# Performance work log

Measured on AMD Instinct MI355X. Metric: run time of the kernel, lower is better.

## Reference

```python
import jax, jax.numpy as jnp
import numpy as np

N_G, E_G = 76800, 307200   # gg: line graph over bonds
N_L, E_L = 38400, 153600   # lg: atom graph; E_L == 2*N_G
B = 64                     # number of molecules (equal-sized subgraphs)
H = 8                      # attention heads
BOND, ATOM, IN_E, FE1 = 40, 92, 10, 36


def _egat_layer(nfeats, efeats, src, dst, N, W_node, b_node, W_ni, W_nj, W_fij, attn, bias, Fn, Fe):
    # edge scores: gather + add (u_add_v) + edge proj + bias, leaky_relu
    f_edge = (nfeats @ W_ni)[src] + (nfeats @ W_nj)[dst] + efeats @ W_fij + bias
    f_out = jax.nn.leaky_relu(f_edge).reshape(-1, H, Fe)         # [E,H,Fe]
    e = jnp.einsum('ehf,hf->eh', f_out, attn)                     # [E,H]
    # edge softmax over incoming edges of each destination node
    m = jax.lax.stop_gradient(jax.ops.segment_max(e, dst, num_segments=N))
    ex = jnp.exp(e - m[dst])
    a = ex / jax.ops.segment_sum(ex, dst, num_segments=N)[dst]    # [E,H]
    h = (nfeats @ W_node + b_node).reshape(-1, H, Fn)             # [N,H,Fn]
    h_out = jax.ops.segment_sum(h[src] * a[:, :, None], dst, num_segments=N)
    return h_out, f_out


def setup_inputs() -> dict:
    key = jax.random.key(0)
    ks = iter(jax.random.split(key, 64))
    def lin(i, o):
        return jax.random.normal(next(ks), (i, o), jnp.float32) * (1.0 / np.sqrt(i))
    inp = {}
    inp['gg_src'] = jax.random.randint(next(ks), (E_G,), 0, N_G, jnp.int32)
    inp['gg_dst'] = jnp.concatenate([jnp.arange(N_G, dtype=jnp.int32),
                                     jax.random.randint(next(ks), (E_G - N_G,), 0, N_G, jnp.int32)])
    inp['gg_nfeat'] = jax.random.normal(next(ks), (N_G, BOND), jnp.float32)
    inp['gg_efeat'] = jax.random.normal(next(ks), (E_G, IN_E), jnp.float32)
    inp['lg_src'] = jax.random.randint(next(ks), (E_L,), 0, N_L, jnp.int32)
    inp['lg_dst'] = jnp.concatenate([jnp.arange(N_L, dtype=jnp.int32),
                                     jax.random.randint(next(ks), (E_L - N_L,), 0, N_L, jnp.int32)])
    inp['lg_nfeat'] = jax.random.normal(next(ks), (N_L, ATOM), jnp.float32)
    inp['lg_efeat'] = jax.random.normal(next(ks), (E_L, BOND), jnp.float32)
    # layer1 (on gg): in_node=BOND, in_edge=IN_E, out_node=BOND, out_edge=FE1
    inp['W_node1'] = lin(BOND, H * BOND); inp['b_node1'] = jnp.zeros((H * BOND,), jnp.float32)
    inp['W_ni1'] = lin(BOND, H * FE1); inp['W_nj1'] = lin(BOND, H * FE1)
    inp['W_fij1'] = lin(IN_E, H * FE1)
    inp['attn1'] = jax.random.normal(next(ks), (H, FE1), jnp.float32) * 0.1
    inp['bias1'] = jnp.zeros((H * FE1,), jnp.float32)
    # layers 2a/2b (on lg): in_node=ATOM, in_edge=BOND, out_node=ATOM, out_edge=BOND
    for sfx in ('2a', '2b'):
        inp['W_node' + sfx] = lin(ATOM, H * ATOM); inp['b_node' + sfx] = jnp.zeros((H * ATOM,), jnp.float32)
        inp['W_ni' + sfx] = lin(ATOM, H * BOND); inp['W_nj' + sfx] = lin(ATOM, H * BOND)
        inp['W_fij' + sfx] = lin(BOND, H * BOND)
        inp['attn' + sfx] = jax.random.normal(next(ks), (H, BOND), jnp.float32) * 0.1
        inp['bias' + sfx] = jnp.zeros((H * BOND,), jnp.float32)
    # Readout: Linear(128,128) + Sigmoid + Linear(128,1) + Sigmoid
    inp['Wr1'] = lin(ATOM + FE1, 128); inp['br1'] = jnp.zeros((128,), jnp.float32)
    inp['Wr2'] = lin(128, 1); inp['br2'] = jnp.zeros((1,), jnp.float32)
    return inp


def reference(gg_src, gg_dst, gg_nfeat, gg_efeat, lg_src, lg_dst, lg_nfeat, lg_efeat,
              W_node1, b_node1, W_ni1, W_nj1, W_fij1, attn1, bias1,
              W_node2a, b_node2a, W_ni2a, W_nj2a, W_fij2a, attn2a, bias2a,
              W_node2b, b_node2b, W_ni2b, W_nj2b, W_fij2b, attn2b, bias2b,
              Wr1, br1, Wr2, br2):
    # stage 1: EGAT on gg, then sum over heads
    n1, e1 = _egat_layer(gg_nfeat, gg_efeat, gg_src, gg_dst, N_G,
                         W_node1, b_node1, W_ni1, W_nj1, W_fij1, attn1, bias1, BOND, FE1)
    y2n = n1.sum(axis=1)       # [N_G, BOND]
    y22 = e1.sum(axis=1)       # [E_G, FE1]
    # each gg-node feature repeated twice, added to lg edge features
    ef = jnp.repeat(y2n, 2, axis=0) + lg_efeat   # [E_L, BOND]
    nf = lg_nfeat
    nf, e2 = _egat_layer(nf, ef, lg_src, lg_dst, N_L,
                         W_node2a, b_node2a, W_ni2a, W_nj2a, W_fij2a, attn2a, bias2a, ATOM, BOND)
    nf = nf.sum(axis=1); ef = e2.sum(axis=1)
    nf, e2 = _egat_layer(nf, ef, lg_src, lg_dst, N_L,
                         W_node2b, b_node2b, W_ni2b, W_nj2b, W_fij2b, attn2b, bias2b, ATOM, BOND)
    nf = nf.sum(axis=1)
    # per-subgraph average pooling (equal-size subgraphs -> reshape mean).
    # NOTE: original pool_subgraphs(y_22, gg) slices an edge-indexed tensor by node
    # counts (upstream quirk); reproduced exactly by taking the first N_G rows.
    y1 = nf.reshape(B, N_L // B, ATOM).mean(axis=1)          # [B, ATOM]
    y2 = y22[:N_G].reshape(B, N_G // B, FE1).mean(axis=1)    # [B, FE1]
    y = jnp.concatenate([y1, y2], axis=1)                     # [B, 128]
    h = jax.nn.sigmoid(y @ Wr1 + br1)
    return jax.nn.sigmoid(h @ Wr2 + br2)                      # [B, 1]
```

## Files before the change

### kernel.cpp

```cpp
#include <hip/hip_runtime.h>
#include <math.h>

#define NG 76800
#define EG 307200
#define NL 38400
#define EL 153600
#define NB 64
#define NH 8

typedef __attribute__((ext_vector_type(8))) short bf16x8;
typedef __attribute__((ext_vector_type(4))) float f32x4;
typedef unsigned short u16;

__device__ __forceinline__ float sigmoidf(float x) { return 1.f / (1.f + expf(-x)); }
__device__ __forceinline__ u16 f2bf(float x) {
    unsigned u = __float_as_uint(x);
    return (u16)((u + 0x7FFFu + ((u >> 16) & 1u)) >> 16);
}
__device__ __forceinline__ float bf2f(u16 v) { return __uint_as_float(((unsigned)v) << 16); }

__global__ __launch_bounds__(256) void convert_pad_kernel(const float* __restrict__ src,
                                                          u16* __restrict__ dst,
                                                          int M, int K, int Kpad) {
    int i = blockIdx.x * 256 + threadIdx.x;
    if (i >= M * Kpad) return;
    int m = i / Kpad, k = i - m * Kpad;
    dst[i] = (k < K) ? f2bf(src[(size_t)m * K + k]) : (u16)0;
}

__global__ __launch_bounds__(256) void wtrans_kernel(const float* __restrict__ W, int ldw,
                                                     u16* __restrict__ dst,
                                                     int K, int N, int Nalloc, int Kpad) {
    int i = blockIdx.x * 256 + threadIdx.x;
    if (i >= Nalloc * Kpad) return;
    int n = i / Kpad, k = i - n * Kpad;
    dst[i] = (n < N && k < K) ? f2bf(W[(size_t)k * ldw + n]) : (u16)0;
}

__global__ __launch_bounds__(256) void wtrans_hp_kernel(const float* __restrict__ W, int ldw,
                                                        u16* __restrict__ dst,
                                                        int K, int Kpad) {
    int i = blockIdx.x * 256 + threadIdx.x;
    if (i >= 320 * Kpad) return;
    int n = i / Kpad, k = i - n * Kpad;
    int hh = n / 40, f = n - hh * 40;
    float v = (k < K && f < 36) ? W[(size_t)k * ldw + hh * 36 + f] : 0.f;
    dst[i] = f2bf(v);
}

__global__ __launch_bounds__(256) void meta_kernel(const float* __restrict__ attn1,
                                                   const float* __restrict__ bias1,
                                                   const float* __restrict__ b2a,
                                                   const float* __restrict__ b2b,
                                                   float* __restrict__ attn_p1,
                                                   float* __restrict__ bias_cat1,
                                                   float* __restrict__ bias_cat2a,
                                                   float* __restrict__ bias_cat2b) {
    int i = blockIdx.x * 256 + threadIdx.x;
    if (i < 320) {
        int hh = i / 40, f = i - hh * 40;
        attn_p1[i] = (f < 36) ? attn1[hh * 36 + f] : 0.f;
    } else if (i < 960) {
        int j = i - 320;
        float v = 0.f;
        if (j < 320) {
            int hh = j / 40, f = j - hh * 40;
            v = (f < 36) ? bias1[hh * 36 + f] : 0.f;
        }
        bias_cat1[j] = v;
    } else if (i < 1600) {
        int j = i - 960;
        bias_cat2a[j] = (j < 320) ? b2a[j] : 0.f;
    } else if (i < 2240) {
        int j = i - 1600;
        bias_cat2b[j] = (j < 320) ? b2b[j] : 0.f;
    }
}

template <int KPAD>
__global__ __launch_bounds__(256) void gemm_bf_kernel(const u16* __restrict__ A,
                                                      const u16* __restrict__ Wt,
                                                      const float* __restrict__ bias,
                                                      u16* __restrict__ C, int Ncols,
                                                      int Nstride) {
    __shared__ u16 st[4][16 * 72];
    const int m0 = blockIdx.x * 64;
    const int n0 = blockIdx.y * 64;
    const int wv = threadIdx.x >> 6;
    const int lane = threadIdx.x & 63;
    const int q = lane >> 4;
    const int mr = lane & 15;

    const u16* Arow = A + (size_t)(m0 + wv * 16 + mr) * KPAD;
    f32x4 acc[4];
#pragma unroll
    for (int t = 0; t < 4; ++t) acc[t] = (f32x4){0.f, 0.f, 0.f, 0.f};

#pragma unroll
    for (int k0 = 0; k0 < KPAD; k0 += 32) {
        bf16x8 af = *(const bf16x8*)(Arow + k0 + q * 8);
#pragma unroll
        for (int t = 0; t < 4; ++t) {
            bf16x8 bv = *(const bf16x8*)(Wt + (size_t)(n0 + t * 16 + mr) * KPAD + k0 + q * 8);
            acc[t] = __builtin_amdgcn_mfma_f32_16x16x32_bf16(af, bv, acc[t], 0, 0, 0);
        }
    }

    u16* myst = st[wv];
#pragma unroll
    for (int t = 0; t < 4; ++t) {
        const int colme = n0 + t * 16 + mr;
        const float bb = (bias && colme < Ncols) ? bias[colme] : 0.f;
#pragma unroll
        for (int r = 0; r < 4; ++r)
            myst[(q * 4 + r) * 72 + t * 16 + mr] = f2bf(acc[t][r] + bb);
    }
    const int rrow = lane >> 3;
    const int rcol = (lane & 7) * 8;
    bf16x8 v0 = *(const bf16x8*)(myst + rrow * 72 + rcol);
    bf16x8 v1 = *(const bf16x8*)(myst + (rrow + 8) * 72 + rcol);
    const int gcol = n0 + rcol;
    if (gcol < Ncols) {
        const int grow = m0 + wv * 16 + rrow;
        *(bf16x8*)(C + (size_t)grow * Nstride + gcol) = v0;
        *(bf16x8*)(C + (size_t)(grow + 8) * Nstride + gcol) = v1;
    }
}

__global__ __launch_bounds__(256) void ef2a_kernel(const float* __restrict__ lg_ef,
                                                   const float* __restrict__ y2n,
                                                   u16* __restrict__ dst) {
    int i = blockIdx.x * 256 + threadIdx.x;
    if (i >= EL * 64) return;
    int e = i >> 6, c = i & 63;
    dst[i] = (c < 40) ? f2bf(lg_ef[(size_t)e * 40 + c] + y2n[(size_t)(e >> 1) * 40 + c]) : (u16)0;
}

template <int KPAD, int FSMODE>
__global__ __launch_bounds__(256) void pe_edge_kernel(
    const u16* __restrict__ A,
    const u16* __restrict__ Wt,
    const int* __restrict__ src, const int* __restrict__ dst,
    const u16* __restrict__ Pn,
    const float* __restrict__ attn,
    float* __restrict__ esc,
    void* __restrict__ fsum,
    int e0, int CH, int fsumE) {
    __shared__ u16 pe[32][328];
    const int wv = threadIdx.x >> 6;
    const int lane = threadIdx.x & 63;
    const int q = lane >> 4;
    const int mr = lane & 15;
    const int m0 = blockIdx.x * 32;

    {
        const int rg0 = (wv & 1) * 16;
        const int t0 = (wv >> 1) * 10;
        const u16* Arow = A + (size_t)(m0 + rg0 + mr) * KPAD;
        f32x4 acc[10];
#pragma unroll
        for (int t = 0; t < 10; ++t) acc[t] = (f32x4){0.f, 0.f, 0.f, 0.f};
#pragma unroll
        for (int k0 = 0; k0 < KPAD; k0 += 32) {
            bf16x8 af = *(const bf16x8*)(Arow + k0 + q * 8);
#pragma unroll
            for (int t = 0; t < 10; ++t) {
                bf16x8 bv = *(const bf16x8*)(Wt + (size_t)((t0 + t) * 16 + mr) * KPAD + k0 + q * 8);
                acc[t] = __builtin_amdgcn_mfma_f32_16x16x32_bf16(af, bv, acc[t], 0, 0, 0);
            }
        }
#pragma unroll
        for (int t = 0; t < 10; ++t)
#pragma unroll
            for (int r = 0; r < 4; ++r)
                pe[rg0 + q * 4 + r][(t0 + t) * 16 + mr] = f2bf(acc[t][r]);
    }
    __syncthreads();

    const int lc = (lane < 40) ? lane : 39;
    const int h = lc / 5, o = lc - h * 5;
    const int c = h * 40 + o * 8;
    const bool act = (lane < 40);

    float attn_r[8];
#pragma unroll
    for (int j = 0; j < 8; ++j) attn_r[j] = attn[c + j];

    const int row0 = wv * 8;
    int e = e0 + m0 + row0;
    int s = src[e], d = dst[e];
    bf16x8 api = *(const bf16x8*)(Pn + (size_t)s * 640 + c);
    bf16x8 apj = *(const bf16x8*)(Pn + (size_t)d * 640 + 320 + c);

#pragma unroll
    for (int ei = 0; ei < 8; ++ei) {
        bf16x8 napi, napj;
        if (ei < 7) {
            const int ne = e + 1;
            const int ns = src[ne], nd = dst[ne];
            napi = *(const bf16x8*)(Pn + (size_t)ns * 640 + c);
            napj = *(const bf16x8*)(Pn + (size_t)nd * 640 + 320 + c);
        }
        const int row = row0 + ei;
        bf16x8 ape = *(const bf16x8*)(&pe[row][c]);

        float v[8];
        float ehp = 0.f;
#pragma unroll
        for (int j = 0; j < 8; ++j) {
            float x = bf2f((u16)api[j]) + bf2f((u16)apj[j]) + bf2f((u16)ape[j]);
            x = x > 0.f ? x : 0.01f * x;
            v[j] = x;
            ehp += x * attn_r[j];
        }
        float eh = 0.f;
#pragma unroll
        for (int k = 0; k < 5; ++k) eh += __shfl(ehp, h * 5 + k, 64);
        if (act && o == 0) esc[(size_t)e * 8 + h] = eh;

        if (FSMODE != 0 && e < fsumE) {
#pragma unroll
            for (int m = 4; m >= 1; m >>= 1) {
                const int p = (h ^ m) * 5 + o;
#pragma unroll
                for (int j = 0; j < 8; ++j) v[j] += __shfl(v[j], p, 64);
            }
            if (act && h == 0) {
#pragma unroll
                for (int j = 0; j < 8; ++j) {
                    const int f = o * 8 + j;
                    if (FSMODE == 1) {
                        if (f < 36) ((float*)fsum)[(size_t)e * 36 + f] = v[j];
                    } else {
                        ((u16*)fsum)[(size_t)e * 64 + f] = f2bf(v[j]);
                    }
                }
            }
        }
        if (ei < 7) {
            api = napi;
            apj = napj;
        }
        ++e;
    }
}

__global__ __launch_bounds__(256) void hist_kernel(const int* __restrict__ dst,
                                                   int* __restrict__ cnt, int E) {
    int i = blockIdx.x * 256 + threadIdx.x;
    if (i < E) atomicAdd(&cnt[dst[i]], 1);
}

__global__ __launch_bounds__(1024) void scan_block_kernel(const int* __restrict__ cnt,
                                                          int* __restrict__ excl,
                                                          int* __restrict__ bsum, int N) {
    __shared__ int sd[1024];
    const int tid = threadIdx.x;
    const int i = blockIdx.x * 1024 + tid;
    int v = (i < N) ? cnt[i] : 0;
    sd[tid] = v;
    __syncthreads();
    for (int off = 1; off < 1024; off <<= 1) {
        int t = (tid >= off) ? sd[tid - off] : 0;
        __syncthreads();
        sd[tid] += t;
        __syncthreads();
    }
    if (i < N) excl[i] = sd[tid] - v;
    if (tid == 1023) bsum[blockIdx.x] = sd[1023];
}

__global__ void scan_top_kernel(int* __restrict__ bsum, int nblk) {
    if (threadIdx.x == 0 && blockIdx.x == 0) {
        int run = 0;
        for (int b = 0; b < nblk; ++b) {
            int t = bsum[b];
            bsum[b] = run;
            run += t;
        }
    }
}

__global__ __launch_bounds__(256) void scan_add_kernel(int* __restrict__ row_ptr,
                                                       const int* __restrict__ bsum,
                                                       int N, int E) {
    int i = blockIdx.x * 256 + threadIdx.x;
    if (i < N) row_ptr[i] += bsum[i >> 10];
    if (i == 0) row_ptr[N] = E;
}

__global__ __launch_bounds__(256) void scatter_kernel(const int* __restrict__ dst,
                                                      const int* __restrict__ src,
                                                      const int* __restrict__ row_ptr,
                                                      int* __restrict__ cur,
                                                      int* __restrict__ eidx,
                                                      int* __restrict__ srcs, int E) {
    int i = blockIdx.x * 256 + threadIdx.x;
    if (i < E) {
        int d = dst[i];
        int pos = row_ptr[d] + atomicAdd(&cur[d], 1);
        eidx[pos] = i;
        srcs[pos] = src[i];
    }
}

template <int GH>
__global__ __launch_bounds__(256) void csr_softmax_kernel(
    const int* __restrict__ row_ptr, const int* __restrict__ eidx,
    const float* __restrict__ esc, float* __restrict__ wcsr, int N) {
    constexpr int NS = 64 / GH;
    const int wid = threadIdx.x >> 6;
    const int lane = threadIdx.x & 63;
    const int nid = blockIdx.x * 4 + wid;
    if (nid >= N) return;
    const int r0 = row_ptr[nid], r1 = row_ptr[nid + 1];
    const int h = lane & (GH - 1);
    const int slot = lane / GH;

    float mx = -1e30f;
    for (int i = r0 + slot; i < r1; i += NS)
        mx = fmaxf(mx, esc[(size_t)eidx[i] * GH + h]);
#pragma unroll
    for (int m = GH; m < 64; m <<= 1) mx = fmaxf(mx, __shfl_xor(mx, m, 64));

    float den = 0.f;
    for (int i = r0 + slot; i < r1; i += NS)
        den += expf(esc[(size_t)eidx[i] * GH + h] - mx);
#pragma unroll
    for (int m = GH; m < 64; m <<= 1) den += __shfl_xor(den, m, 64);
    const float rden = 1.f / den;

    for (int i = r0 + slot; i < r1; i += NS)
        wcsr[(size_t)i * GH + h] = expf(esc[(size_t)eidx[i] * GH + h] - mx) * rden;
}

template <int Fn, int GH, int OM, int STR>
__global__ __launch_bounds__(256) void node_agg_kernel(
    const int* __restrict__ row_ptr,
    const int* __restrict__ srcs,
    const float* __restrict__ wcsr,
    const u16* __restrict__ Pnode,
    void* __restrict__ outp, int N) {
    constexpr int PAIRS = Fn / 2;
    const int wid = threadIdx.x >> 6;
    const int lane = threadIdx.x & 63;
    const int nid = blockIdx.x * 4 + wid;
    if (nid >= N) return;
    const int r0 = row_ptr[nid], r1 = row_ptr[nid + 1];
    const int col = 2 * lane;
    const bool act = (lane < PAIRS);

    float a0 = 0.f, a1 = 0.f;
    for (int i = r0; i < r1; i += 4) {
        const u16* prs[4];
        float wv[4][GH];
#pragma unroll
        for (int b = 0; b < 4; ++b) {
            const int ii = (i + b < r1) ? (i + b) : (r1 - 1);
            prs[b] = Pnode + (size_t)srcs[ii] * STR;
            const float live = (i + b < r1) ? 1.f : 0.f;
            const float* wp = wcsr + (size_t)ii * GH;
#pragma unroll
            for (int hh = 0; hh < GH; ++hh) wv[b][hh] = wp[hh] * live;
        }
        if (act) {
            unsigned pv[4][GH];
#pragma unroll
            for (int b = 0; b < 4; ++b)
#pragma unroll
                for (int hh = 0; hh < GH; ++hh)
                    pv[b][hh] = *(const unsigned*)(prs[b] + hh * Fn + col);
#pragma unroll
            for (int b = 0; b < 4; ++b)
#pragma unroll
                for (int hh = 0; hh < GH; ++hh) {
                    a0 += wv[b][hh] * bf2f((u16)(pv[b][hh] & 0xFFFFu));
                    a1 += wv[b][hh] * bf2f((u16)(pv[b][hh] >> 16));
                }
        }
    }
    if (OM == 0) {
        if (act) {
            float* op = (float*)outp + (size_t)nid * Fn + col;
            op[0] = a0;
            op[1] = a1;
        }
    } else {
        unsigned* ob = (unsigned*)((u16*)outp + (size_t)nid * 96);
        if (act) {
            unsigned pk = (unsigned)f2bf(a0) | ((unsigned)f2bf(a1) << 16);
            ob[lane] = pk;
        } else if (lane < 48) {
            ob[lane] = 0u;
        }
    }
}

__global__ __launch_bounds__(256) void readout_kernel(const u16* __restrict__ nfb,
                                                      const float* __restrict__ y22p,
                                                      const float* __restrict__ Wr1,
                                                      const float* __restrict__ br1,
                                                      const float* __restrict__ Wr2,
                                                      const float* __restrict__ br2,
                                                      float* __restrict__ out) {
    const int b = blockIdx.x;
    const int t = threadIdx.x;
    __shared__ float y[128];
    __shared__ float hh[128];
    __shared__ float red[128];
    if (t < 92) {
        float s = 0.f;
        const u16* base = nfb + (size_t)b * 600 * 96 + t;
        for (int i = 0; i < 600; ++i) s += bf2f(base[(size_t)i * 96]);
        y[t] = s * (1.f / 600.f);
    } else if (t >= 128 && t < 164) {
        int f = t - 128;
        float s = 0.f;
        const float* base = y22p + (size_t)b * 1200 * 36 + f;
        for (int i = 0; i < 1200; ++i) s += base[(size_t)i * 36];
        y[92 + f] = s * (1.f / 1200.f);
    }
    __syncthreads();
    if (t < 128) {
        float s = br1[t];
        for (int c = 0; c < 128; ++c) s += y[c] * Wr1[(size_t)c * 128 + t];
        hh[t] = sigmoidf(s);
    }
    __syncthreads();
    if (t < 128) red[t] = hh[t] * Wr2[t];
    __syncthreads();
    for (int k = 64; k > 0; k >>= 1) {
        if (t < k) red[t] += red[t + k];
        __syncthreads();
    }
    if (t == 0) out[b] = sigmoidf(red[0] + br2[0]);
}

static inline int cdiv(int a, int b) { return (a + b - 1) / b; }

extern "C" void kernel_launch(void* const* d_in, const int* in_sizes, int n_in,
                              void* d_out, int out_size, void* d_ws, size_t ws_size,
                              hipStream_t stream) {
    const int* gg_src = (const int*)d_in[0];
    const int* gg_dst = (const int*)d_in[1];
    const float* gg_nf = (const float*)d_in[2];
    const float* gg_ef = (const float*)d_in[3];
    const int* lg_src = (const int*)d_in[4];
    const int* lg_dst = (const int*)d_in[5];
    const float* lg_nf = (const float*)d_in[6];
    const float* lg_ef = (const float*)d_in[7];
    const float* W_node1 = (const float*)d_in[8];
    const float* b_node1 = (const float*)d_in[9];
    const float* W_ni1 = (const float*)d_in[10];
    const float* W_nj1 = (const float*)d_in[11];
    const float* W_fij1 = (const float*)d_in[12];
    const float* attn1 = (const float*)d_in[13];
    const float* bias1 = (const float*)d_in[14];
    const float* W_node2a = (const float*)d_in[15];
    const float* b_node2a = (const float*)d_in[16];
    const float* W_ni2a = (const float*)d_in[17];
    const float* W_nj2a = (const float*)d_in[18];
    const float* W_fij2a = (const float*)d_in[19];
    const float* attn2a = (const float*)d_in[20];
    const float* bias2a = (const float*)d_in[21];
    const float* W_node2b = (const float*)d_in[22];
    const float* b_node2b = (const float*)d_in[23];
    const float* W_ni2b = (const float*)d_in[24];
    const float* W_nj2b = (const float*)d_in[25];
    const float* W_fij2b = (const float*)d_in[26];
    const float* attn2b = (const float*)d_in[27];
    const float* bias2b = (const float*)d_in[28];
    const float* Wr1 = (const float*)d_in[29];
    const float* br1 = (const float*)d_in[30];
    const float* Wr2 = (const float*)d_in[31];
    const float* br2 = (const float*)d_in[32];
    float* out = (float*)d_out;

    char* ws = (char*)d_ws;
    size_t off = 0;
    auto take = [&](size_t bytes) {
        size_t o = off;
        off += (bytes + 255) & ~(size_t)255;
        return (void*)(ws + o);
    };
    float* y2n = (float*)take((size_t)NG * 40 * 4);
    float* y22p = (float*)take((size_t)NG * 36 * 4);
    float* esc = (float*)take((size_t)EG * 8 * 4);
    float* wcsr = (float*)take((size_t)EG * 8 * 4);
    int* gg_row = (int*)take((size_t)(NG + 1) * 4);
    int* gg_eidx = (int*)take((size_t)EG * 4);
    int* gg_srcs = (int*)take((size_t)EG * 4);
    int* gg_cnt = (int*)take((size_t)NG * 4);
    int* lg_row = (int*)take((size_t)(NL + 1) * 4);
    int* lg_eidx = (int*)take((size_t)EL * 4);
    int* lg_srcs = (int*)take((size_t)EL * 4);
    int* lg_cnt = (int*)take((size_t)NL * 4);
    int* bsum = (int*)take((size_t)128 * 4);
    u16* gg_nf_bf = (u16*)take((size_t)NG * 64 * 2);
    u16* gg_ef_bf = (u16*)take((size_t)EG * 32 * 2);
    u16* lg_nf_bf = (u16*)take((size_t)NL * 96 * 2);
    u16* nfa_bf = (u16*)take((size_t)NL * 96 * 2);
    u16* nfb_bf = (u16*)take((size_t)NL * 96 * 2);
    u16* ef_shared = (u16*)take((size_t)EL * 64 * 2);
    u16* wt_ninj1 = (u16*)take((size_t)640 * 64 * 2);
    u16* wt_node1 = (u16*)take((size_t)320 * 64 * 2);
    u16* wt_fij1 = (u16*)take((size_t)320 * 32 * 2);
    u16* wt_ninj2a = (u16*)take((size_t)640 * 96 * 2);
    u16* wt_ninj2b = (u16*)take((size_t)640 * 96 * 2);
    u16* wt_fij2a = (u16*)take((size_t)320 * 64 * 2);
    u16* wt_fij2b = (u16*)take((size_t)320 * 64 * 2);
    u16* wt_node2a = (u16*)take((size_t)768 * 96 * 2);
    u16* wt_node2b = (u16*)take((size_t)768 * 96 * 2);
    float* attn_p1 = (float*)take((size_t)320 * 4);
    float* bias_cat1 = (float*)take((size_t)640 * 4);
    float* bias_cat2a = (float*)take((size_t)640 * 4);
    float* bias_cat2b = (float*)take((size_t)640 * 4);
    u16* slab = (u16*)take((size_t)NG * 640 * 2);

    auto cvt = [&](const float* s, u16* d, int M, int K, int Kpad) {
        convert_pad_kernel<<<cdiv(M * Kpad, 256), 256, 0, stream>>>(s, d, M, K, Kpad);
    };
    auto wtr = [&](const float* W, int ldw, u16* d, int K, int N, int Nalloc, int Kpad) {
        wtrans_kernel<<<cdiv(Nalloc * Kpad, 256), 256, 0, stream>>>(W, ldw, d, K, N, Nalloc, Kpad);
    };
    auto build_csr = [&](const int* dst, const int* src, int* row_ptr, int* eidx, int* srcs,
                         int* cnt, int N, int E) {
        hipMemsetAsync(cnt, 0, (size_t)N * 4, stream);
        hist_kernel<<<cdiv(E, 256), 256, 0, stream>>>(dst, cnt, E);
        int nblk = cdiv(N, 1024);
        scan_block_kernel<<<nblk, 1024, 0, stream>>>(cnt, row_ptr, bsum, N);
        scan_top_kernel<<<1, 64, 0, stream>>>(bsum, nblk);
        scan_add_kernel<<<cdiv(N, 256), 256, 0, stream>>>(row_ptr, bsum, N, E);
        hipMemsetAsync(cnt, 0, (size_t)N * 4, stream);
        scatter_kernel<<<cdiv(E, 256), 256, 0, stream>>>(dst, src, row_ptr, cnt, eidx, srcs, E);
    };

    build_csr(gg_dst, gg_src, gg_row, gg_eidx, gg_srcs, gg_cnt, NG, EG);
    build_csr(lg_dst, lg_src, lg_row, lg_eidx, lg_srcs, lg_cnt, NL, EL);

    cvt(gg_nf, gg_nf_bf, NG, 40, 64);
    cvt(gg_ef, gg_ef_bf, EG, 10, 32);
    cvt(lg_nf, lg_nf_bf, NL, 92, 96);
    wtrans_hp_kernel<<<cdiv(320 * 64, 256), 256, 0, stream>>>(W_ni1, 288, wt_ninj1, 40, 64);
    wtrans_hp_kernel<<<cdiv(320 * 64, 256), 256, 0, stream>>>(W_nj1, 288, wt_ninj1 + 320 * 64, 40, 64);
    wtrans_hp_kernel<<<cdiv(320 * 32, 256), 256, 0, stream>>>(W_fij1, 288, wt_fij1, 10, 32);
    wtr(W_node1, 320, wt_node1, 40, 320, 320, 64);
    wtr(W_ni2a, 320, wt_ninj2a, 92, 320, 320, 96);
    wtr(W_nj2a, 320, wt_ninj2a + 320 * 96, 92, 320, 320, 96);
    wtr(W_ni2b, 320, wt_ninj2b, 92, 320, 320, 96);
    wtr(W_nj2b, 320, wt_ninj2b + 320 * 96, 92, 320, 320, 96);
    wtr(W_fij2a, 320, wt_fij2a, 40, 320, 320, 64);
    wtr(W_fij2b, 320, wt_fij2b, 40, 320, 320, 64);
    wtr(W_node2a, 736, wt_node2a, 92, 736, 768, 96);
    wtr(W_node2b, 736, wt_node2b, 92, 736, 768, 96);
    meta_kernel<<<cdiv(2240, 256), 256, 0, stream>>>(attn1, bias1, bias2a, bias2b,
                                                     attn_p1, bias_cat1, bias_cat2a, bias_cat2b);

    {
        u16* Pn1 = slab;
        gemm_bf_kernel<64><<<dim3(NG / 64, 10), 256, 0, stream>>>(
            gg_nf_bf, wt_ninj1, bias_cat1, Pn1, 640, 640);
        pe_edge_kernel<32, 1><<<EG / 32, 256, 0, stream>>>(
            gg_ef_bf, wt_fij1, gg_src, gg_dst, Pn1, attn_p1, esc, y22p, 0, EG, NG);
        csr_softmax_kernel<8><<<NG / 4, 256, 0, stream>>>(gg_row, gg_eidx, esc, wcsr, NG);
        u16* Pnode1 = slab;
        gemm_bf_kernel<64><<<dim3(NG / 64, 5), 256, 0, stream>>>(
            gg_nf_bf, wt_node1, b_node1, Pnode1, 320, 320);
        node_agg_kernel<40, 8, 0, 320><<<NG / 4, 256, 0, stream>>>(gg_row, gg_srcs, wcsr,
                                                                   Pnode1, y2n, NG);
    }

    ef2a_kernel<<<cdiv(EL * 64, 256), 256, 0, stream>>>(lg_ef, y2n, ef_shared);

    for (int layer = 0; layer < 2; ++layer) {
        const bool a = (layer == 0);
        const u16* nf_in = a ? lg_nf_bf : nfa_bf;
        const u16* Wninj = a ? wt_ninj2a : wt_ninj2b;
        const u16* Wfij = a ? wt_fij2a : wt_fij2b;
        const u16* Wnode = a ? wt_node2a : wt_node2b;
        const float* bn = a ? b_node2a : b_node2b;
        const float* bcat = a ? bias_cat2a : bias_cat2b;
        const float* at = a ? attn2a : attn2b;
        u16* nf_out = a ? nfa_bf : nfb_bf;

        u16* Pn2 = slab;
        gemm_bf_kernel<96><<<dim3(NL / 64, 10), 256, 0, stream>>>(nf_in, Wninj, bcat, Pn2, 640, 640);
        if (a)
            pe_edge_kernel<64, 2><<<EL / 32, 256, 0, stream>>>(
                ef_shared, Wfij, lg_src, lg_dst, Pn2, at, esc, ef_shared, 0, EL, EL);
        else
            pe_edge_kernel<64, 0><<<EL / 32, 256, 0, stream>>>(
                ef_shared, Wfij, lg_src, lg_dst, Pn2, at, esc, nullptr, 0, EL, 0);
        csr_softmax_kernel<8><<<NL / 4, 256, 0, stream>>>(lg_row, lg_eidx, esc, wcsr, NL);
        u16* Pnode2 = slab;
        gemm_bf_kernel<96><<<dim3(NL / 64, 12), 256, 0, stream>>>(nf_in, Wnode, bn, Pnode2, 736, 768);
        node_agg_kernel<92, 8, 1, 768><<<NL / 4, 256, 0, stream>>>(lg_row, lg_srcs, wcsr,
                                                                   Pnode2, nf_out, NL);
    }

    readout_kernel<<<NB, 256, 0, stream>>>(nfb_bf, y22p, Wr1, br1, Wr2, br2, out);
}
```

Before: 980.5 us.

## Fuse node projections into edge kernel by gathering raw node features per edge

```diff
diff --git a/kernel.cpp b/kernel.cpp
--- a/kernel.cpp
+++ b/kernel.cpp
@@ -136,16 +136,21 @@
     dst[i] = (c < 40) ? f2bf(lg_ef[(size_t)e * 40 + c] + y2n[(size_t)(e >> 1) * 40 + c]) : (u16)0;
 }
 
-template <int KPAD, int FSMODE>
+template <int KN, int KE, int FSMODE>
 __global__ __launch_bounds__(256) void pe_edge_kernel(
-    const u16* __restrict__ A,
-    const u16* __restrict__ Wt,
+    const u16* __restrict__ nf,
+    const u16* __restrict__ ef,
+    const u16* __restrict__ wt_ni,
+    const u16* __restrict__ wt_nj,
+    const u16* __restrict__ wt_fij,
+    const float* __restrict__ bias320,
     const int* __restrict__ src, const int* __restrict__ dst,
-    const u16* __restrict__ Pn,
     const float* __restrict__ attn,
     float* __restrict__ esc,
     void* __restrict__ fsum,
-    int e0, int CH, int fsumE) {
+    int fsumE) {
+    constexpr int SN = KN / 32;
+    constexpr int SE = KE / 32;
     __shared__ u16 pe[32][328];
     const int wv = threadIdx.x >> 6;
     const int lane = threadIdx.x & 63;
@@ -156,24 +161,43 @@
     {
         const int rg0 = (wv & 1) * 16;
         const int t0 = (wv >> 1) * 10;
-        const u16* Arow = A + (size_t)(m0 + rg0 + mr) * KPAD;
-        f32x4 acc[10];
-#pragma unroll
-        for (int t = 0; t < 10; ++t) acc[t] = (f32x4){0.f, 0.f, 0.f, 0.f};
-#pragma unroll
-        for (int k0 = 0; k0 < KPAD; k0 += 32) {
-            bf16x8 af = *(const bf16x8*)(Arow + k0 + q * 8);
-#pragma unroll
-            for (int t = 0; t < 10; ++t) {
-                bf16x8 bv = *(const bf16x8*)(Wt + (size_t)((t0 + t) * 16 + mr) * KPAD + k0 + q * 8);
-                acc[t] = __builtin_amdgcn_mfma_f32_16x16x32_bf16(af, bv, acc[t], 0, 0, 0);
+        const int er = m0 + rg0 + mr;
+        const u16* pS = nf + (size_t)src[er] * KN;
+        const u16* pD = nf + (size_t)dst[er] * KN;
+        const u16* pE = ef + (size_t)er * KE;
+        bf16x8 afs[SN], afd[SN], afe[SE];
+#pragma unroll
+        for (int k = 0; k < SN; ++k) {
+            afs[k] = *(const bf16x8*)(pS + k * 32 + q * 8);
+            afd[k] = *(const bf16x8*)(pD + k * 32 + q * 8);
+        }
+#pragma unroll
+        for (int k = 0; k < SE; ++k) afe[k] = *(const bf16x8*)(pE + k * 32 + q * 8);
+
+#pragma unroll
+        for (int t = 0; t < 10; ++t) {
+            const int nrow = (t0 + t) * 16 + mr;
+            const float b = bias320[nrow];
+            f32x4 a = (f32x4){b, b, b, b};
+#pragma unroll
+            for (int k = 0; k < SN; ++k) {
+                bf16x8 bv = *(const bf16x8*)(wt_ni + (size_t)nrow * KN + k * 32 + q * 8);
+                a = __builtin_amdgcn_mfma_f32_16x16x32_bf16(afs[k], bv, a, 0, 0, 0);
             }
-        }
-#pragma unroll
-        for (int t = 0; t < 10; ++t)
+#pragma unroll
+            for (int k = 0; k < SN; ++k) {
+                bf16x8 bv = *(const bf16x8*)(wt_nj + (size_t)nrow * KN + k * 32 + q * 8);
+                a = __builtin_amdgcn_mfma_f32_16x16x32_bf16(afd[k], bv, a, 0, 0, 0);
+            }
+#pragma unroll
+            for (int k = 0; k < SE; ++k) {
+                bf16x8 bv = *(const bf16x8*)(wt_fij + (size_t)nrow * KE + k * 32 + q * 8);
+                a = __builtin_amdgcn_mfma_f32_16x16x32_bf16(afe[k], bv, a, 0, 0, 0);
+            }
 #pragma unroll
             for (int r = 0; r < 4; ++r)
-                pe[rg0 + q * 4 + r][(t0 + t) * 16 + mr] = f2bf(acc[t][r]);
+                pe[rg0 + q * 4 + r][(t0 + t) * 16 + mr] = f2bf(a[r]);
+        }
     }
     __syncthreads();
 
@@ -186,29 +210,17 @@
 #pragma unroll
     for (int j = 0; j < 8; ++j) attn_r[j] = attn[c + j];
 
-    const int row0 = wv * 8;
-    int e = e0 + m0 + row0;
-    int s = src[e], d = dst[e];
-    bf16x8 api = *(const bf16x8*)(Pn + (size_t)s * 640 + c);
-    bf16x8 apj = *(const bf16x8*)(Pn + (size_t)d * 640 + 320 + c);
-
 #pragma unroll
     for (int ei = 0; ei < 8; ++ei) {
-        bf16x8 napi, napj;
-        if (ei < 7) {
-            const int ne = e + 1;
-            const int ns = src[ne], nd = dst[ne];
-            napi = *(const bf16x8*)(Pn + (size_t)ns * 640 + c);
-            napj = *(const bf16x8*)(Pn + (size_t)nd * 640 + 320 + c);
-        }
-        const int row = row0 + ei;
+        const int row = wv * 8 + ei;
+        const int e = m0 + row;
         bf16x8 ape = *(const bf16x8*)(&pe[row][c]);
 
         float v[8];
         float ehp = 0.f;
 #pragma unroll
         for (int j = 0; j < 8; ++j) {
-            float x = bf2f((u16)api[j]) + bf2f((u16)apj[j]) + bf2f((u16)ape[j]);
+            float x = bf2f((u16)ape[j]);
             x = x > 0.f ? x : 0.01f * x;
             v[j] = x;
             ehp += x * attn_r[j];
@@ -237,11 +249,6 @@
                 }
             }
         }
-        if (ei < 7) {
-            api = napi;
-            apj = napj;
-        }
-        ++e;
     }
 }
 
@@ -515,7 +522,9 @@
     float* bias_cat1 = (float*)take((size_t)640 * 4);
     float* bias_cat2a = (float*)take((size_t)640 * 4);
     float* bias_cat2b = (float*)take((size_t)640 * 4);
-    u16* slab = (u16*)take((size_t)NG * 640 * 2);
+    u16* slab = (u16*)take((size_t)NL * 768 * 2 > (size_t)NG * 320 * 2
+                               ? (size_t)NL * 768 * 2
+                               : (size_t)NG * 320 * 2);
 
     auto cvt = [&](const float* s, u16* d, int M, int K, int Kpad) {
         convert_pad_kernel<<<cdiv(M * Kpad, 256), 256, 0, stream>>>(s, d, M, K, Kpad);
@@ -557,11 +566,9 @@
                                                      attn_p1, bias_cat1, bias_cat2a, bias_cat2b);
 
     {
-        u16* Pn1 = slab;
-        gemm_bf_kernel<64><<<dim3(NG / 64, 10), 256, 0, stream>>>(
-            gg_nf_bf, wt_ninj1, bias_cat1, Pn1, 640, 640);
-        pe_edge_kernel<32, 1><<<EG / 32, 256, 0, stream>>>(
-            gg_ef_bf, wt_fij1, gg_src, gg_dst, Pn1, attn_p1, esc, y22p, 0, EG, NG);
+        pe_edge_kernel<64, 32, 1><<<EG / 32, 256, 0, stream>>>(
+            gg_nf_bf, gg_ef_bf, wt_ninj1, wt_ninj1 + 320 * 64, wt_fij1, bias_cat1,
+            gg_src, gg_dst, attn_p1, esc, y22p, NG);
         csr_softmax_kernel<8><<<NG / 4, 256, 0, stream>>>(gg_row, gg_eidx, esc, wcsr, NG);
         u16* Pnode1 = slab;
         gemm_bf_kernel<64><<<dim3(NG / 64, 5), 256, 0, stream>>>(
@@ -583,14 +590,14 @@
         const float* at = a ? attn2a : attn2b;
         u16* nf_out = a ? nfa_bf : nfb_bf;
 
-        u16* Pn2 = slab;
-        gemm_bf_kernel<96><<<dim3(NL / 64, 10), 256, 0, stream>>>(nf_in, Wninj, bcat, Pn2, 640, 640);
         if (a)
-            pe_edge_kernel<64, 2><<<EL / 32, 256, 0, stream>>>(
-                ef_shared, Wfij, lg_src, lg_dst, Pn2, at, esc, ef_shared, 0, EL, EL);
+            pe_edge_kernel<96, 64, 2><<<EL / 32, 256, 0, stream>>>(
+                nf_in, ef_shared, Wninj, Wninj + 320 * 96, Wfij, bcat,
+                lg_src, lg_dst, at, esc, ef_shared, EL);
         else
-            pe_edge_kernel<64, 0><<<EL / 32, 256, 0, stream>>>(
-                ef_shared, Wfij, lg_src, lg_dst, Pn2, at, esc, nullptr, 0, EL, 0);
+            pe_edge_kernel<96, 64, 0><<<EL / 32, 256, 0, stream>>>(
+                nf_in, ef_shared, Wninj, Wninj + 320 * 96, Wfij, bcat,
+                lg_src, lg_dst, at, esc, nullptr, 0);
         csr_softmax_kernel<8><<<NL / 4, 256, 0, stream>>>(lg_row, lg_eidx, esc, wcsr, NL);
         u16* Pnode2 = slab;
         gemm_bf_kernel<96><<<dim3(NL / 64, 12), 256, 0, stream>>>(nf_in, Wnode, bn, Pnode2, 736, 768);
```

Measured after the change: 1.095 ms. 1.12x slower.

## Aggregate raw node features per head before projecting, folding head-sum into GEMM

Applied to the files above, without the earlier changes.

```diff
diff --git a/kernel.cpp b/kernel.cpp
--- a/kernel.cpp
+++ b/kernel.cpp
@@ -46,6 +46,28 @@
     int hh = n / 40, f = n - hh * 40;
     float v = (k < K && f < 36) ? W[(size_t)k * ldw + hh * 36 + f] : 0.f;
     dst[i] = f2bf(v);
+}
+
+__global__ __launch_bounds__(256) void wtrans_cat_kernel(const float* __restrict__ W, int ldw,
+                                                         u16* __restrict__ dst,
+                                                         int Fin, int Fout, int Nalloc, int KIN) {
+    int i = blockIdx.x * 256 + threadIdx.x;
+    if (i >= Nalloc * KIN) return;
+    int n = i / KIN, k = i - n * KIN;
+    int h = k / Fin, f = k - h * Fin;
+    float v = (n < Fout) ? W[(size_t)f * ldw + h * Fout + n] : 0.f;
+    dst[i] = f2bf(v);
+}
+
+__global__ __launch_bounds__(256) void bias_headsum_kernel(const float* __restrict__ b,
+                                                           float* __restrict__ outp,
+                                                           int Fout, int H, int Npad) {
+    int i = blockIdx.x * 256 + threadIdx.x;
+    if (i >= Npad) return;
+    float s = 0.f;
+    if (i < Fout)
+        for (int h = 0; h < H; ++h) s += b[h * Fout + i];
+    outp[i] = s;
 }
 
 __global__ __launch_bounds__(256) void meta_kernel(const float* __restrict__ attn1,
@@ -128,12 +150,13 @@
 }
 
 __global__ __launch_bounds__(256) void ef2a_kernel(const float* __restrict__ lg_ef,
-                                                   const float* __restrict__ y2n,
+                                                   const u16* __restrict__ y2n,
                                                    u16* __restrict__ dst) {
     int i = blockIdx.x * 256 + threadIdx.x;
     if (i >= EL * 64) return;
     int e = i >> 6, c = i & 63;
-    dst[i] = (c < 40) ? f2bf(lg_ef[(size_t)e * 40 + c] + y2n[(size_t)(e >> 1) * 40 + c]) : (u16)0;
+    dst[i] = (c < 40) ? f2bf(lg_ef[(size_t)e * 40 + c] + bf2f(y2n[(size_t)(e >> 1) * 40 + c]))
+                      : (u16)0;
 }
 
 template <int KPAD, int FSMODE>
@@ -334,13 +357,13 @@
         wcsr[(size_t)i * GH + h] = expf(esc[(size_t)eidx[i] * GH + h] - mx) * rden;
 }
 
-template <int Fn, int GH, int OM, int STR>
-__global__ __launch_bounds__(256) void node_agg_kernel(
+template <int Fn, int GH, int NFS>
+__global__ __launch_bounds__(256) void node_agg_raw_kernel(
     const int* __restrict__ row_ptr,
     const int* __restrict__ srcs,
     const float* __restrict__ wcsr,
-    const u16* __restrict__ Pnode,
-    void* __restrict__ outp, int N) {
+    const u16* __restrict__ nf,
+    u16* __restrict__ agg, int N) {
     constexpr int PAIRS = Fn / 2;
     const int wid = threadIdx.x >> 6;
     const int lane = threadIdx.x & 63;
@@ -350,48 +373,44 @@
     const int col = 2 * lane;
     const bool act = (lane < PAIRS);
 
-    float a0 = 0.f, a1 = 0.f;
+    float a0[GH], a1[GH];
+#pragma unroll
+    for (int h = 0; h < GH; ++h) { a0[h] = 0.f; a1[h] = 0.f; }
+
     for (int i = r0; i < r1; i += 4) {
         const u16* prs[4];
         float wv[4][GH];
 #pragma unroll
         for (int b = 0; b < 4; ++b) {
             const int ii = (i + b < r1) ? (i + b) : (r1 - 1);
-            prs[b] = Pnode + (size_t)srcs[ii] * STR;
+            prs[b] = nf + (size_t)srcs[ii] * NFS;
             const float live = (i + b < r1) ? 1.f : 0.f;
             const float* wp = wcsr + (size_t)ii * GH;
 #pragma unroll
-            for (int hh = 0; hh < GH; ++hh) wv[b][hh] = wp[hh] * live;
+            for (int h = 0; h < GH; ++h) wv[b][h] = wp[h] * live;
         }
         if (act) {
-            unsigned pv[4][GH];
-#pragma unroll
-            for (int b = 0; b < 4; ++b)
-#pragma unroll
-                for (int hh = 0; hh < GH; ++hh)
-                    pv[b][hh] = *(const unsigned*)(prs[b] + hh * Fn + col);
-#pragma unroll
-            for (int b = 0; b < 4; ++b)
-#pragma unroll
-                for (int hh = 0; hh < GH; ++hh) {
-                    a0 += wv[b][hh] * bf2f((u16)(pv[b][hh] & 0xFFFFu));
-                    a1 += wv[b][hh] * bf2f((u16)(pv[b][hh] >> 16));
+            unsigned pv[4];
+#pragma unroll
+            for (int b = 0; b < 4; ++b) pv[b] = *(const unsigned*)(prs[b] + col);
+#pragma unroll
+            for (int b = 0; b < 4; ++b) {
+                const float lo = bf2f((u16)(pv[b] & 0xFFFFu));
+                const float hi = bf2f((u16)(pv[b] >> 16));
+#pragma unroll
+                for (int h = 0; h < GH; ++h) {
+                    a0[h] += wv[b][h] * lo;
+                    a1[h] += wv[b][h] * hi;
                 }
-        }
-    }
-    if (OM == 0) {
-        if (act) {
-            float* op = (float*)outp + (size_t)nid * Fn + col;
-            op[0] = a0;
-            op[1] = a1;
-        }
-    } else {
-        unsigned* ob = (unsigned*)((u16*)outp + (size_t)nid * 96);
-        if (act) {
-            unsigned pk = (unsigned)f2bf(a0) | ((unsigned)f2bf(a1) << 16);
-            ob[lane] = pk;
-        } else if (lane < 48) {
-            ob[lane] = 0u;
+            }
+        }
+    }
+    if (act) {
+        u16* ob = agg + (size_t)nid * (GH * Fn);
+#pragma unroll
+        for (int h = 0; h < GH; ++h) {
+            unsigned pk = (unsigned)f2bf(a0[h]) | ((unsigned)f2bf(a1[h]) << 16);
+            *(unsigned*)(ob + h * Fn + col) = pk;
         }
     }
 }
@@ -483,7 +502,7 @@
         off += (bytes + 255) & ~(size_t)255;
         return (void*)(ws + o);
     };
-    float* y2n = (float*)take((size_t)NG * 40 * 4);
+    u16* y2n = (u16*)take((size_t)NG * 40 * 2);
     float* y22p = (float*)take((size_t)NG * 36 * 4);
     float* esc = (float*)take((size_t)EG * 8 * 4);
     float* wcsr = (float*)take((size_t)EG * 8 * 4);
@@ -503,14 +522,17 @@
     u16* nfb_bf = (u16*)take((size_t)NL * 96 * 2);
     u16* ef_shared = (u16*)take((size_t)EL * 64 * 2);
     u16* wt_ninj1 = (u16*)take((size_t)640 * 64 * 2);
-    u16* wt_node1 = (u16*)take((size_t)320 * 64 * 2);
     u16* wt_fij1 = (u16*)take((size_t)320 * 32 * 2);
     u16* wt_ninj2a = (u16*)take((size_t)640 * 96 * 2);
     u16* wt_ninj2b = (u16*)take((size_t)640 * 96 * 2);
     u16* wt_fij2a = (u16*)take((size_t)320 * 64 * 2);
     u16* wt_fij2b = (u16*)take((size_t)320 * 64 * 2);
-    u16* wt_node2a = (u16*)take((size_t)768 * 96 * 2);
-    u16* wt_node2b = (u16*)take((size_t)768 * 96 * 2);
+    u16* wt_cat1 = (u16*)take((size_t)64 * 320 * 2);
+    u16* wt_cat2a = (u16*)take((size_t)128 * 736 * 2);
+    u16* wt_cat2b = (u16*)take((size_t)128 * 736 * 2);
+    float* bsum1 = (float*)take((size_t)64 * 4);
+    float* bsum2a = (float*)take((size_t)128 * 4);
+    float* bsum2b = (float*)take((size_t)128 * 4);
     float* attn_p1 = (float*)take((size_t)320 * 4);
     float* bias_cat1 = (float*)take((size_t)640 * 4);
     float* bias_cat2a = (float*)take((size_t)640 * 4);
@@ -544,15 +566,18 @@
     wtrans_hp_kernel<<<cdiv(320 * 64, 256), 256, 0, stream>>>(W_ni1, 288, wt_ninj1, 40, 64);
     wtrans_hp_kernel<<<cdiv(320 * 64, 256), 256, 0, stream>>>(W_nj1, 288, wt_ninj1 + 320 * 64, 40, 64);
     wtrans_hp_kernel<<<cdiv(320 * 32, 256), 256, 0, stream>>>(W_fij1, 288, wt_fij1, 10, 32);
-    wtr(W_node1, 320, wt_node1, 40, 320, 320, 64);
     wtr(W_ni2a, 320, wt_ninj2a, 92, 320, 320, 96);
     wtr(W_nj2a, 320, wt_ninj2a + 320 * 96, 92, 320, 320, 96);
     wtr(W_ni2b, 320, wt_ninj2b, 92, 320, 320, 96);
     wtr(W_nj2b, 320, wt_ninj2b + 320 * 96, 92, 320, 320, 96);
     wtr(W_fij2a, 320, wt_fij2a, 40, 320, 320, 64);
     wtr(W_fij2b, 320, wt_fij2b, 40, 320, 320, 64);
-    wtr(W_node2a, 736, wt_node2a, 92, 736, 768, 96);
-    wtr(W_node2b, 736, wt_node2b, 92, 736, 768, 96);
+    wtrans_cat_kernel<<<cdiv(64 * 320, 256), 256, 0, stream>>>(W_node1, 320, wt_cat1, 40, 40, 64, 320);
+    wtrans_cat_kernel<<<cdiv(128 * 736, 256), 256, 0, stream>>>(W_node2a, 736, wt_cat2a, 92, 92, 128, 736);
+    wtrans_cat_kernel<<<cdiv(128 * 736, 256), 256, 0, stream>>>(W_node2b, 736, wt_cat2b, 92, 92, 128, 736);
+    bias_headsum_kernel<<<1, 256, 0, stream>>>(b_node1, bsum1, 40, 8, 64);
+    bias_headsum_kernel<<<1, 256, 0, stream>>>(b_node2a, bsum2a, 92, 8, 128);
+    bias_headsum_kernel<<<1, 256, 0, stream>>>(b_node2b, bsum2b, 92, 8, 128);
     meta_kernel<<<cdiv(2240, 256), 256, 0, stream>>>(attn1, bias1, bias2a, bias2b,
                                                      attn_p1, bias_cat1, bias_cat2a, bias_cat2b);
 
@@ -563,11 +588,11 @@
         pe_edge_kernel<32, 1><<<EG / 32, 256, 0, stream>>>(
             gg_ef_bf, wt_fij1, gg_src, gg_dst, Pn1, attn_p1, esc, y22p, 0, EG, NG);
         csr_softmax_kernel<8><<<NG / 4, 256, 0, stream>>>(gg_row, gg_eidx, esc, wcsr, NG);
-        u16* Pnode1 = slab;
-        gemm_bf_kernel<64><<<dim3(NG / 64, 5), 256, 0, stream>>>(
-            gg_nf_bf, wt_node1, b_node1, Pnode1, 320, 320);
-        node_agg_kernel<40, 8, 0, 320><<<NG / 4, 256, 0, stream>>>(gg_row, gg_srcs, wcsr,
-                                                                   Pnode1, y2n, NG);
+        u16* agg1 = slab;
+        node_agg_raw_kernel<40, 8, 64><<<NG / 4, 256, 0, stream>>>(gg_row, gg_srcs, wcsr,
+                                                                   gg_nf_bf, agg1, NG);
+        gemm_bf_kernel<320><<<dim3(NG / 64, 1), 256, 0, stream>>>(
+            agg1, wt_cat1, bsum1, y2n, 40, 40);
     }
 
     ef2a_kernel<<<cdiv(EL * 64, 256), 256, 0, stream>>>(lg_ef, y2n, ef_shared);
@@ -577,8 +602,8 @@
         const u16* nf_in = a ? lg_nf_bf : nfa_bf;
         const u16* Wninj = a ? wt_ninj2a : wt_ninj2b;
         const u16* Wfij = a ? wt_fij2a : wt_fij2b;
-        const u16* Wnode = a ? wt_node2a : wt_node2b;
-        const float* bn = a ? b_node2a : b_node2b;
+        const u16* Wcat = a ? wt_cat2a : wt_cat2b;
+        const float* bs = a ? bsum2a : bsum2b;
         const float* bcat = a ? bias_cat2a : bias_cat2b;
         const float* at = a ? attn2a : attn2b;
         u16* nf_out = a ? nfa_bf : nfb_bf;
@@ -592,10 +617,11 @@
             pe_edge_kernel<64, 0><<<EL / 32, 256, 0, stream>>>(
                 ef_shared, Wfij, lg_src, lg_dst, Pn2, at, esc, nullptr, 0, EL, 0);
         csr_softmax_kernel<8><<<NL / 4, 256, 0, stream>>>(lg_row, lg_eidx, esc, wcsr, NL);
-        u16* Pnode2 = slab;
-        gemm_bf_kernel<96><<<dim3(NL / 64, 12), 256, 0, stream>>>(nf_in, Wnode, bn, Pnode2, 736, 768);
-        node_agg_kernel<92, 8, 1, 768><<<NL / 4, 256, 0, stream>>>(lg_row, lg_srcs, wcsr,
-                                                                   Pnode2, nf_out, NL);
+        u16* agg2 = slab;
+        node_agg_raw_kernel<92, 8, 96><<<NL / 4, 256, 0, stream>>>(lg_row, lg_srcs, wcsr,
+                                                                   nf_in, agg2, NL);
+        gemm_bf_kernel<736><<<dim3(NL / 64, 2), 256, 0, stream>>>(
+            agg2, Wcat, bs, nf_out, 96, 96);
     }
 
     readout_kernel<<<NB, 256, 0, stream>>>(nfb_bf, y22p, Wr1, br1, Wr2, br2, out);
```

After: 973.6 us. No clear change (-0.7%).
